# Optimization experiments

Hardware: AMD Instinct MI355X
Metric: run time of the kernel (lower is better)

## Reference

```python
import jax, jax.numpy as jnp
import numpy as np


def setup_inputs() -> dict:
    key = jax.random.key(0)
    k1, k2, k3, k4 = jax.random.split(key, 4)
    b, c, h, w = 4, 256, 64, 64
    Fq_l = jax.random.normal(k1, (b, c, h, w), dtype=jnp.float32)
    Fp_l = jax.random.normal(k2, (b, c, h, w), dtype=jnp.float32)
    # 1x1 conv: weight [out=c//2, in=c], bias [c//2]
    W = jax.random.normal(k3, (c // 2, c), dtype=jnp.float32) * (1.0 / np.sqrt(c))
    bias = jax.random.normal(k4, (c // 2,), dtype=jnp.float32) * 0.01
    return {"Fq_l": Fq_l, "Fp_l": Fp_l, "W": W, "bias": bias}


def reference(Fq_l, Fp_l, W, bias):
    b, c, h, w = Fq_l.shape
    hw = h * w
    # 1x1 conv == per-pixel linear projection
    q = jnp.einsum('oc,bchw->bohw', W, Fq_l) + bias[None, :, None, None]
    p = jnp.einsum('oc,bchw->bohw', W, Fp_l) + bias[None, :, None, None]
    qf = q.reshape(b, -1, hw)  # [b, c/2, hw]
    pf = p.reshape(b, -1, hw)
    qf = qf / jnp.linalg.norm(qf, axis=1, keepdims=True)
    pf = pf / jnp.linalg.norm(pf, axis=1, keepdims=True)
    # cosine similarity, [b, hw, hw]
    sim = jnp.einsum('bcn,bcm->bnm', qf, pf)
    idx = jnp.argmax(sim, axis=-1)  # [b, hw]
    Fp_flat = Fp_l.reshape(b, c, hw)
    aligned = jnp.take_along_axis(Fp_flat, idx[:, None, :], axis=2)  # [b, c, hw]
    return aligned.reshape(b, c, h, w)
```

## Files before the change

kernel.cpp:

```cpp
#include <hip/hip_runtime.h>

#define HW 4096
#define LCAP 1536

typedef short bf16x8 __attribute__((ext_vector_type(8)));
typedef float f32x16 __attribute__((ext_vector_type(16)));

__device__ __forceinline__ ushort f2bf_rne(float f) {
    unsigned u = __float_as_uint(f);
    return (ushort)((u + 0x7FFFu + ((u >> 16) & 1u)) >> 16);
}

__global__ __launch_bounds__(256) void transpose_w_kernel(
    const float* __restrict__ Wm, float* __restrict__ Wt)
{
    const int o = blockIdx.x;
    const int c = threadIdx.x;
    Wt[c * 128 + o] = Wm[o * 256 + c];
}

__global__ __launch_bounds__(256) void proj_kernel(
    const float* __restrict__ Fq, const float* __restrict__ Fp,
    const float* __restrict__ Wt, const float* __restrict__ bias,
    float* __restrict__ Qt, float* __restrict__ Pt,
    ushort* __restrict__ Qpk, ushort* __restrict__ Ppk,
    float* __restrict__ qnorm)
{
    __shared__ float Ws[64][128];
    __shared__ float Xs[64][64];
    __shared__ float psum[16][68];

    const int tid = threadIdx.x;
    const int z  = blockIdx.z;
    const float* __restrict__ X = z ? Fp : Fq;
    const int b  = blockIdx.y;
    const int n0 = blockIdx.x * 64;
    const int og = tid >> 4;
    const int ng = tid & 15;

    float acc[4][8];
    #pragma unroll
    for (int i = 0; i < 4; ++i)
        #pragma unroll
        for (int j = 0; j < 8; ++j) acc[i][j] = 0.f;

    for (int cc = 0; cc < 4; ++cc) {
        __syncthreads();
        {
            const float4* src = (const float4*)(Wt + (size_t)cc * 64 * 128);
            float4* dst = (float4*)Ws;
            #pragma unroll
            for (int it = 0; it < 8; ++it) dst[it * 256 + tid] = src[it * 256 + tid];
        }
        #pragma unroll
        for (int it = 0; it < 4; ++it) {
            int f = it * 256 + tid;
            int r = f >> 4, n4 = f & 15;
            *(float4*)&Xs[r][n4 * 4] =
                *(const float4*)&X[(size_t)(b * 256 + cc * 64 + r) * HW + n0 + n4 * 4];
        }
        __syncthreads();

        for (int r = 0; r < 64; ++r) {
            float4 w0 = *(const float4*)&Ws[r][og * 8];
            float4 w1 = *(const float4*)&Ws[r][og * 8 + 4];
            float4 xv = *(const float4*)&Xs[r][ng * 4];
            float wa[8] = {w0.x, w0.y, w0.z, w0.w, w1.x, w1.y, w1.z, w1.w};
            float xa[4] = {xv.x, xv.y, xv.z, xv.w};
            #pragma unroll
            for (int i = 0; i < 4; ++i)
                #pragma unroll
                for (int j = 0; j < 8; ++j)
                    acc[i][j] += wa[j] * xa[i];
        }
    }

    {
        float4 b0 = *(const float4*)&bias[og * 8];
        float4 b1 = *(const float4*)&bias[og * 8 + 4];
        float ba[8] = {b0.x, b0.y, b0.z, b0.w, b1.x, b1.y, b1.z, b1.w};
        #pragma unroll
        for (int i = 0; i < 4; ++i)
            #pragma unroll
            for (int j = 0; j < 8; ++j) acc[i][j] += ba[j];
    }

    #pragma unroll
    for (int i = 0; i < 4; ++i) {
        float s = 0.f;
        #pragma unroll
        for (int j = 0; j < 8; ++j) s += acc[i][j] * acc[i][j];
        psum[og][ng * 4 + i] = s;
    }
    __syncthreads();
    float tot[4];
    #pragma unroll
    for (int i = 0; i < 4; ++i) {
        float s = 0.f;
        #pragma unroll
        for (int g = 0; g < 16; ++g) s += psum[g][ng * 4 + i];
        tot[i] = s;
    }

    if (z) {
        #pragma unroll
        for (int i = 0; i < 4; ++i) {
            float s = 1.0f / sqrtf(tot[i]);
            #pragma unroll
            for (int j = 0; j < 8; ++j) acc[i][j] *= s;
        }
    } else if (og == 0) {
        #pragma unroll
        for (int i = 0; i < 4; ++i)
            qnorm[b * HW + n0 + ng * 4 + i] = sqrtf(tot[i]);
    }

    {
        float* __restrict__ T = z ? Pt : Qt;
        #pragma unroll
        for (int i = 0; i < 4; ++i) {
            size_t tb = ((size_t)b * HW + n0 + ng * 4 + i) * 128 + og * 8;
            *(float4*)&T[tb]     = make_float4(acc[i][0], acc[i][1], acc[i][2], acc[i][3]);
            *(float4*)&T[tb + 4] = make_float4(acc[i][4], acc[i][5], acc[i][6], acc[i][7]);
        }
    }
    {
        ushort* __restrict__ PK = z ? Ppk : Qpk;
        const int ks = og >> 1;
        #pragma unroll
        for (int i = 0; i < 4; ++i) {
            const int na  = n0 + ng * 4 + i;
            const int t32 = na >> 5;
            const int lt  = (na & 31) + 32 * (og & 1);
            ushort u[8];
            #pragma unroll
            for (int k = 0; k < 8; ++k) u[k] = f2bf_rne(acc[i][k]);
            size_t pk = ((((size_t)b * 128 + t32) * 8 + ks) * 64 + lt) * 8;
            uint4 w;
            w.x = (unsigned)u[0] | ((unsigned)u[1] << 16);
            w.y = (unsigned)u[2] | ((unsigned)u[3] << 16);
            w.z = (unsigned)u[4] | ((unsigned)u[5] << 16);
            w.w = (unsigned)u[6] | ((unsigned)u[7] << 16);
            *(uint4*)&PK[pk] = w;
        }
    }
}

__global__ __launch_bounds__(256, 4) void sim_sketch_kernel(
    const ushort* __restrict__ Qpk, const ushort* __restrict__ Ppk,
    const float* __restrict__ qnorm,
    float* __restrict__ Vmax, unsigned char* __restrict__ SK,
    unsigned char* __restrict__ CM)
{
    __shared__ ushort Bs[16384];

    const int tid  = threadIdx.x;
    const int lane = tid & 63;
    const int w    = tid >> 6;
    const int nb   = blockIdx.x;
    const int b    = blockIdx.y;
    const int ms   = blockIdx.z;
    const int hi   = lane >> 5;

    {
        const uint4* src = (const uint4*)(Ppk + ((size_t)(b * 128 + ms * 4)) * 4096);
        uint4* dst = (uint4*)Bs;
        #pragma unroll
        for (int it = 0; it < 8; ++it) dst[it * 256 + tid] = src[it * 256 + tid];
    }

    const ushort* __restrict__ qbase =
        Qpk + ((size_t)(b * 128 + nb * 4)) * 4096 + (size_t)lane * 8;
    bf16x8 qf[8];
    #pragma unroll
    for (int ks = 0; ks < 8; ++ks)
        qf[ks] = *(const bf16x8*)(qbase + (w * 8 + ks) * 512);

    float rq[16];
    #pragma unroll
    for (int r = 0; r < 16; ++r) {
        int nl_ = (r & 3) + 8 * (r >> 2) + 4 * hi;
        rq[r] = 256.0f / qnorm[b * HW + nb * 128 + w * 32 + nl_];
    }

    const size_t g16f = (size_t)b * 256 + (size_t)(nb * 4 + w) * 2 + hi;
    const int mb0 = ms * 128 + (lane & 31);

    float bestv[16];
    #pragma unroll
    for (int r = 0; r < 16; ++r) bestv[r] = -1e30f;

    __syncthreads();

    #pragma unroll 2
    for (int mtl = 0; mtl < 4; ++mtl) {
        f32x16 acc;
        #pragma unroll
        for (int r = 0; r < 16; ++r) acc[r] = 0.f;
        #pragma unroll
        for (int ks = 0; ks < 8; ++ks) {
            bf16x8 bb = *(const bf16x8*)&Bs[((mtl * 8 + ks) * 64 + lane) * 8];
            acc = __builtin_amdgcn_mfma_f32_32x32x16_bf16(qf[ks], bb, acc, 0, 0, 0);
        }
        #pragma unroll
        for (int r = 0; r < 16; ++r)
            bestv[r] = fmaxf(bestv[r], acc[r]);

        float x[16];
        #pragma unroll
        for (int r = 0; r < 16; ++r) x[r] = acc[r] * rq[r];

        float c0 = fmaxf(fmaxf(fmaxf(x[0], x[1]), fmaxf(x[2], x[3])),
                         fmaxf(fmaxf(x[4], x[5]), fmaxf(x[6], x[7])));
        float c1 = fmaxf(fmaxf(fmaxf(x[8], x[9]), fmaxf(x[10], x[11])),
                         fmaxf(fmaxf(x[12], x[13]), fmaxf(x[14], x[15])));
        int cmi = (int)(fmaxf(c0, c1) + 0.5f) + 1;
        cmi = cmi < 0 ? 0 : (cmi > 255 ? 255 : cmi);

        unsigned dw[4] = {0u, 0u, 0u, 0u};
        #pragma unroll
        for (int r = 0; r < 16; ++r) {
#if __has_builtin(__builtin_amdgcn_cvt_pk_u8_f32)
            dw[r >> 2] = (unsigned)__builtin_amdgcn_cvt_pk_u8_f32(
                x[r], (unsigned)(r & 3), (int)dw[r >> 2]);
#else
            int vi = (int)rintf(x[r]);
            vi = vi < 0 ? 0 : (vi > 255 ? 255 : vi);
            dw[r >> 2] |= (unsigned)vi << (8 * (r & 3));
#endif
        }
        const int m = mb0 + mtl * 32;
        uint4 pk;
        pk.x = dw[0]; pk.y = dw[1]; pk.z = dw[2]; pk.w = dw[3];
        *(uint4*)(SK + ((g16f * 4096 + (size_t)m) << 4)) = pk;
        CM[g16f * 4096 + (size_t)m] = (unsigned char)cmi;
    }

    #pragma unroll
    for (int r = 0; r < 16; ++r) {
        float v = bestv[r];
        #pragma unroll
        for (int d = 1; d < 32; d <<= 1)
            v = fmaxf(v, __shfl_xor(v, d, 64));
        if ((lane & 31) == 0) {
            int nl_ = (r & 3) + 8 * (r >> 2) + 4 * hi;
            int na = nb * 128 + w * 32 + nl_;
            Vmax[((size_t)b * HW + na) * 32 + ms] = v;
        }
    }
}

__device__ __noinline__ void dot_one_slow(
    const float* Qsrow, const float* __restrict__ Pt,
    int b, int m, int n, unsigned long long* __restrict__ best)
{
    const float4* __restrict__ pr = (const float4*)&Pt[((size_t)b * HW + m) * 128];
    float acc = 0.f;
    #pragma unroll
    for (int k = 0; k < 32; ++k) {
        float4 pv = pr[k];
        float4 qv = *(const float4*)&Qsrow[k * 4];
        acc += qv.x * pv.x + qv.y * pv.y + qv.z * pv.z + qv.w * pv.w;
    }
    unsigned u = __float_as_uint(acc);
    unsigned kk = (u & 0x80000000u) ? ~u : (u | 0x80000000u);
    unsigned long long key = ((unsigned long long)kk << 32) | (unsigned)(4095 - m);
    atomicMax(&best[(size_t)b * HW + n], key);
}

__global__ __launch_bounds__(256) void scan_rescore_kernel(
    const unsigned char* __restrict__ SK, const unsigned char* __restrict__ CM,
    const float* __restrict__ Vmax, const float* __restrict__ qnorm,
    const float* __restrict__ Qt, const float* __restrict__ Pt,
    unsigned long long* __restrict__ best)
{
    __shared__ float Qs[16][132];
    __shared__ int nlist[16];
    __shared__ int t8s[16];
    __shared__ ushort hl[LCAP];
    __shared__ unsigned lcnt;

    const int fg  = blockIdx.x;
    const int tid = threadIdx.x;
    const int b = fg >> 8, g = fg & 255, t = g >> 1, gs = g & 1;

    if (tid == 0) lcnt = 0u;
    if (tid < 16) {
        int n = t * 32 + (tid & 3) + 8 * (tid >> 2) + 4 * gs;
        nlist[tid] = n;
        best[(size_t)b * HW + n] = 0ull;
        float gmax = -1e30f;
        const float4* vs = (const float4*)&Vmax[((size_t)b * HW + n) * 32];
        #pragma unroll
        for (int s = 0; s < 8; ++s) {
            float4 v = vs[s];
            gmax = fmaxf(gmax, fmaxf(fmaxf(v.x, v.y), fmaxf(v.z, v.w)));
        }
        float qn  = qnorm[b * HW + n];
        float thr = gmax - (0.016f * qn + 1e-6f);
        int tt = (int)floorf(thr * (256.0f / qn)) - 1;
        t8s[tid] = tt < 0 ? 0 : (tt > 255 ? 255 : tt);
    }
    __syncthreads();

    #pragma unroll
    for (int it = 0; it < 2; ++it) {
        int idx = it * 256 + tid;
        int row = idx >> 5, c4 = (idx & 31) * 4;
        *(float4*)&Qs[row][c4] =
            *(const float4*)&Qt[((size_t)b * HW + nlist[row]) * 128 + c4];
    }

    int myt[16];
    #pragma unroll
    for (int j = 0; j < 16; ++j) myt[j] = t8s[j];
    int gmin = myt[0];
    #pragma unroll
    for (int j = 1; j < 16; ++j) gmin = min(gmin, myt[j]);
    __syncthreads();

    const unsigned char* __restrict__ cmrow = CM + ((size_t)fg << 12);
    const unsigned char* __restrict__ skrow = SK + ((size_t)fg << 16);

    #pragma unroll
    for (int it = 0; it < 4; ++it) {
        int m0 = (it * 256 + tid) * 4;
        unsigned cm4 = *(const unsigned*)(cmrow + m0);
        #pragma unroll
        for (int k = 0; k < 4; ++k) {
            int cmv = (int)((cm4 >> (8 * k)) & 255u);
            if (cmv >= gmin) {
                int m = m0 + k;
                uint4 v = *(const uint4*)(skrow + ((size_t)m << 4));
                unsigned wv[4] = {v.x, v.y, v.z, v.w};
                #pragma unroll
                for (int d = 0; d < 4; ++d) {
                    #pragma unroll
                    for (int kk = 0; kk < 4; ++kk) {
                        int bv = (int)((wv[d] >> (8 * kk)) & 255u);
                        int j = d * 4 + kk;
                        if (bv >= myt[j]) {
                            unsigned pos = atomicAdd(&lcnt, 1u);
                            if (pos < LCAP) {
                                hl[pos] = (ushort)((j << 12) | m);
                            } else {
                                dot_one_slow(&Qs[j][0], Pt, b, m, nlist[j], best);
                            }
                        }
                    }
                }
            }
        }
    }

    __syncthreads();
    unsigned cnt = lcnt < LCAP ? lcnt : LCAP;
    for (unsigned p = tid; p < cnt; p += 256) {
        int e = hl[p];
        int j = e >> 12, m = e & 4095;
        const float4* __restrict__ pr = (const float4*)&Pt[((size_t)b * HW + m) * 128];
        float acc = 0.f;
        #pragma unroll
        for (int k = 0; k < 32; ++k) {
            float4 pv = pr[k];
            float4 qv = *(const float4*)&Qs[j][k * 4];
            acc += qv.x * pv.x + qv.y * pv.y + qv.z * pv.z + qv.w * pv.w;
        }
        unsigned u = __float_as_uint(acc);
        unsigned kk = (u & 0x80000000u) ? ~u : (u | 0x80000000u);
        unsigned long long key = ((unsigned long long)kk << 32) | (unsigned)(4095 - m);
        atomicMax(&best[(size_t)b * HW + nlist[j]], key);
    }
}

__global__ __launch_bounds__(256) void gather_kernel(
    const float* __restrict__ Fp, const unsigned long long* __restrict__ best,
    float* __restrict__ out)
{
    __shared__ float row[4096];
    const int blk = blockIdx.x;
    const int c = blk & 255;
    const int b = blk >> 8;
    const int tid = threadIdx.x;

    const float* __restrict__ src = Fp + ((size_t)b * 256 + c) * HW;
    #pragma unroll
    for (int it = 0; it < 4; ++it) {
        int f = it * 256 + tid;
        *(float4*)&row[f * 4] = *(const float4*)&src[f * 4];
    }
    __syncthreads();

    float* __restrict__ dst = out + ((size_t)b * 256 + c) * HW;
    #pragma unroll
    for (int it = 0; it < 16; ++it) {
        int n = it * 256 + tid;
        int m = 4095 - (int)(best[(size_t)b * HW + n] & 0xFFFull);
        dst[n] = row[m];
    }
}

extern "C" void kernel_launch(void* const* d_in, const int* in_sizes, int n_in,
                              void* d_out, int out_size, void* d_ws, size_t ws_size,
                              hipStream_t stream) {
    const float* Fq   = (const float*)d_in[0];
    const float* Fp   = (const float*)d_in[1];
    const float* Wm   = (const float*)d_in[2];
    const float* bias = (const float*)d_in[3];
    float* out = (float*)d_out;

    char* base = (char*)d_ws;
    float*  Qt    = (float*)(base);
    float*  Pt    = (float*)(base + (8u << 20));
    ushort* Qpk   = (ushort*)(base + (16u << 20));
    ushort* Ppk   = (ushort*)(base + (20u << 20));
    unsigned char* SK = (unsigned char*)(base + (24u << 20));
    unsigned char* CM = (unsigned char*)(base + (88u << 20));
    char* x = base + (92u << 20);
    float*  qnorm = (float*)x;              x += 65536;
    float*  Vmax  = (float*)x;              x += 2097152;
    unsigned long long* best = (unsigned long long*)x; x += 131072;
    float*  Wtg   = (float*)x;

    transpose_w_kernel<<<128, 256, 0, stream>>>(Wm, Wtg);
    proj_kernel<<<dim3(64, 4, 2), 256, 0, stream>>>(Fq, Fp, Wtg, bias,
                                                    Qt, Pt, Qpk, Ppk, qnorm);
    sim_sketch_kernel<<<dim3(32, 4, 32), 256, 0, stream>>>(Qpk, Ppk, qnorm,
                                                           Vmax, SK, CM);
    scan_rescore_kernel<<<1024, 256, 0, stream>>>(SK, CM, Vmax, qnorm,
                                                  Qt, Pt, best);
    gather_kernel<<<1024, 256, 0, stream>>>(Fp, best, out);
}
```

Before: 179.6 us.

## Replace float Vmax and column-max sketch with quantized per-tile row max

The sim kernel now writes a compact uint8 per-row, per-tile maximum of the scaled similarity, replacing both the float Vmax array and the per-column CM byte array. The rescore kernel derives each row's threshold as the quantized max minus a fixed margin of 6. It also drops the CM-based column prefilter and instead scans the whole SK sketch with coalesced uint4 loads. This cuts global writes and reads of Vmax and CM, and removes the divergent gather-style SK reads. In exchange it reads all of SK unconditionally, and the threshold now relies on quantized values, which may change how many candidates get rescored.

```diff
diff --git a/kernel.cpp b/kernel.cpp
--- a/kernel.cpp
+++ b/kernel.cpp
@@ -148,9 +148,8 @@
 
 __global__ __launch_bounds__(256, 4) void sim_sketch_kernel(
     const ushort* __restrict__ Qpk, const ushort* __restrict__ Ppk,
-    const float* __restrict__ qnorm,
-    float* __restrict__ Vmax, unsigned char* __restrict__ SK,
-    unsigned char* __restrict__ CM)
+    const float* __restrict__ qnorm, unsigned char* __restrict__ SK,
+    unsigned char* __restrict__ BM)
 {
     __shared__ ushort Bs[16384];
 
@@ -186,9 +185,9 @@
     const size_t g16f = (size_t)b * 256 + (size_t)(nb * 4 + w) * 2 + hi;
     const int mb0 = ms * 128 + (lane & 31);
 
-    float bestv[16];
-    #pragma unroll
-    for (int r = 0; r < 16; ++r) bestv[r] = -1e30f;
+    float xmax[16];
+    #pragma unroll
+    for (int r = 0; r < 16; ++r) xmax[r] = -1e30f;
 
     __syncthreads();
 
@@ -202,29 +201,17 @@
             bf16x8 bb = *(const bf16x8*)&Bs[((mtl * 8 + ks) * 64 + lane) * 8];
             acc = __builtin_amdgcn_mfma_f32_32x32x16_bf16(qf[ks], bb, acc, 0, 0, 0);
         }
-        #pragma unroll
-        for (int r = 0; r < 16; ++r)
-            bestv[r] = fmaxf(bestv[r], acc[r]);
-
-        float x[16];
-        #pragma unroll
-        for (int r = 0; r < 16; ++r) x[r] = acc[r] * rq[r];
-
-        float c0 = fmaxf(fmaxf(fmaxf(x[0], x[1]), fmaxf(x[2], x[3])),
-                         fmaxf(fmaxf(x[4], x[5]), fmaxf(x[6], x[7])));
-        float c1 = fmaxf(fmaxf(fmaxf(x[8], x[9]), fmaxf(x[10], x[11])),
-                         fmaxf(fmaxf(x[12], x[13]), fmaxf(x[14], x[15])));
-        int cmi = (int)(fmaxf(c0, c1) + 0.5f) + 1;
-        cmi = cmi < 0 ? 0 : (cmi > 255 ? 255 : cmi);
 
         unsigned dw[4] = {0u, 0u, 0u, 0u};
         #pragma unroll
         for (int r = 0; r < 16; ++r) {
+            float x = acc[r] * rq[r];
+            xmax[r] = fmaxf(xmax[r], x);
 #if __has_builtin(__builtin_amdgcn_cvt_pk_u8_f32)
             dw[r >> 2] = (unsigned)__builtin_amdgcn_cvt_pk_u8_f32(
-                x[r], (unsigned)(r & 3), (int)dw[r >> 2]);
+                x, (unsigned)(r & 3), (int)dw[r >> 2]);
 #else
-            int vi = (int)rintf(x[r]);
+            int vi = (int)rintf(x);
             vi = vi < 0 ? 0 : (vi > 255 ? 255 : vi);
             dw[r >> 2] |= (unsigned)vi << (8 * (r & 3));
 #endif
@@ -233,20 +220,32 @@
         uint4 pk;
         pk.x = dw[0]; pk.y = dw[1]; pk.z = dw[2]; pk.w = dw[3];
         *(uint4*)(SK + ((g16f * 4096 + (size_t)m) << 4)) = pk;
-        CM[g16f * 4096 + (size_t)m] = (unsigned char)cmi;
     }
 
     #pragma unroll
     for (int r = 0; r < 16; ++r) {
-        float v = bestv[r];
+        float v = xmax[r];
         #pragma unroll
         for (int d = 1; d < 32; d <<= 1)
             v = fmaxf(v, __shfl_xor(v, d, 64));
-        if ((lane & 31) == 0) {
-            int nl_ = (r & 3) + 8 * (r >> 2) + 4 * hi;
-            int na = nb * 128 + w * 32 + nl_;
-            Vmax[((size_t)b * HW + na) * 32 + ms] = v;
-        }
+        xmax[r] = v;
+    }
+    if ((lane & 31) == 0) {
+        unsigned dw[4] = {0u, 0u, 0u, 0u};
+        #pragma unroll
+        for (int r = 0; r < 16; ++r) {
+#if __has_builtin(__builtin_amdgcn_cvt_pk_u8_f32)
+            dw[r >> 2] = (unsigned)__builtin_amdgcn_cvt_pk_u8_f32(
+                xmax[r], (unsigned)(r & 3), (int)dw[r >> 2]);
+#else
+            int vi = (int)rintf(xmax[r]);
+            vi = vi < 0 ? 0 : (vi > 255 ? 255 : vi);
+            dw[r >> 2] |= (unsigned)vi << (8 * (r & 3));
+#endif
+        }
+        uint4 pk;
+        pk.x = dw[0]; pk.y = dw[1]; pk.z = dw[2]; pk.w = dw[3];
+        *(uint4*)(BM + ((g16f * 32 + (size_t)ms) << 4)) = pk;
     }
 }
 
@@ -269,8 +268,7 @@
 }
 
 __global__ __launch_bounds__(256) void scan_rescore_kernel(
-    const unsigned char* __restrict__ SK, const unsigned char* __restrict__ CM,
-    const float* __restrict__ Vmax, const float* __restrict__ qnorm,
+    const unsigned char* __restrict__ SK, const unsigned char* __restrict__ BM,
     const float* __restrict__ Qt, const float* __restrict__ Pt,
     unsigned long long* __restrict__ best)
 {
@@ -289,17 +287,13 @@
         int n = t * 32 + (tid & 3) + 8 * (tid >> 2) + 4 * gs;
         nlist[tid] = n;
         best[(size_t)b * HW + n] = 0ull;
-        float gmax = -1e30f;
-        const float4* vs = (const float4*)&Vmax[((size_t)b * HW + n) * 32];
-        #pragma unroll
-        for (int s = 0; s < 8; ++s) {
-            float4 v = vs[s];
-            gmax = fmaxf(gmax, fmaxf(fmaxf(v.x, v.y), fmaxf(v.z, v.w)));
-        }
-        float qn  = qnorm[b * HW + n];
-        float thr = gmax - (0.016f * qn + 1e-6f);
-        int tt = (int)floorf(thr * (256.0f / qn)) - 1;
-        t8s[tid] = tt < 0 ? 0 : (tt > 255 ? 255 : tt);
+        const unsigned char* __restrict__ bmrow = BM + ((size_t)fg << 9);
+        int mc = 0;
+        #pragma unroll
+        for (int ms = 0; ms < 32; ++ms)
+            mc = max(mc, (int)bmrow[ms * 16 + tid]);
+        int tt = mc - 6;
+        t8s[tid] = tt < 0 ? 0 : tt;
     }
     __syncthreads();
 
@@ -314,39 +308,27 @@
     int myt[16];
     #pragma unroll
     for (int j = 0; j < 16; ++j) myt[j] = t8s[j];
-    int gmin = myt[0];
-    #pragma unroll
-    for (int j = 1; j < 16; ++j) gmin = min(gmin, myt[j]);
-    __syncthreads();
-
-    const unsigned char* __restrict__ cmrow = CM + ((size_t)fg << 12);
-    const unsigned char* __restrict__ skrow = SK + ((size_t)fg << 16);
-
-    #pragma unroll
-    for (int it = 0; it < 4; ++it) {
-        int m0 = (it * 256 + tid) * 4;
-        unsigned cm4 = *(const unsigned*)(cmrow + m0);
-        #pragma unroll
-        for (int k = 0; k < 4; ++k) {
-            int cmv = (int)((cm4 >> (8 * k)) & 255u);
-            if (cmv >= gmin) {
-                int m = m0 + k;
-                uint4 v = *(const uint4*)(skrow + ((size_t)m << 4));
-                unsigned wv[4] = {v.x, v.y, v.z, v.w};
-                #pragma unroll
-                for (int d = 0; d < 4; ++d) {
-                    #pragma unroll
-                    for (int kk = 0; kk < 4; ++kk) {
-                        int bv = (int)((wv[d] >> (8 * kk)) & 255u);
-                        int j = d * 4 + kk;
-                        if (bv >= myt[j]) {
-                            unsigned pos = atomicAdd(&lcnt, 1u);
-                            if (pos < LCAP) {
-                                hl[pos] = (ushort)((j << 12) | m);
-                            } else {
-                                dot_one_slow(&Qs[j][0], Pt, b, m, nlist[j], best);
-                            }
-                        }
+    __syncthreads();
+
+    const uint4* __restrict__ skrow = (const uint4*)(SK + ((size_t)fg << 16));
+
+    #pragma unroll 4
+    for (int it = 0; it < 16; ++it) {
+        const int m = it * 256 + tid;
+        uint4 v = skrow[it * 256 + tid];
+        unsigned wv[4] = {v.x, v.y, v.z, v.w};
+        #pragma unroll
+        for (int d = 0; d < 4; ++d) {
+            #pragma unroll
+            for (int k = 0; k < 4; ++k) {
+                int bv = (int)((wv[d] >> (8 * k)) & 255u);
+                int j = d * 4 + k;
+                if (bv >= myt[j]) {
+                    unsigned pos = atomicAdd(&lcnt, 1u);
+                    if (pos < LCAP) {
+                        hl[pos] = (ushort)((j << 12) | m);
+                    } else {
+                        dot_one_slow(&Qs[j][0], Pt, b, m, nlist[j], best);
                     }
                 }
             }
@@ -415,10 +397,9 @@
     ushort* Qpk   = (ushort*)(base + (16u << 20));
     ushort* Ppk   = (ushort*)(base + (20u << 20));
     unsigned char* SK = (unsigned char*)(base + (24u << 20));
-    unsigned char* CM = (unsigned char*)(base + (88u << 20));
-    char* x = base + (92u << 20);
+    char* x = base + (88u << 20);
+    unsigned char* BM = (unsigned char*)x;  x += 524288;
     float*  qnorm = (float*)x;              x += 65536;
-    float*  Vmax  = (float*)x;              x += 2097152;
     unsigned long long* best = (unsigned long long*)x; x += 131072;
     float*  Wtg   = (float*)x;
 
@@ -426,8 +407,7 @@
     proj_kernel<<<dim3(64, 4, 2), 256, 0, stream>>>(Fq, Fp, Wtg, bias,
                                                     Qt, Pt, Qpk, Ppk, qnorm);
     sim_sketch_kernel<<<dim3(32, 4, 32), 256, 0, stream>>>(Qpk, Ppk, qnorm,
-                                                           Vmax, SK, CM);
-    scan_rescore_kernel<<<1024, 256, 0, stream>>>(SK, CM, Vmax, qnorm,
-                                                  Qt, Pt, best);
+                                                           SK, BM);
+    scan_rescore_kernel<<<1024, 256, 0, stream>>>(SK, BM, Qt, Pt, best);
     gather_kernel<<<1024, 256, 0, stream>>>(Fp, best, out);
 }
```

Measured after the change: 168.8 us. -6.0%, faster.
